# Optimization experiments

Hardware: AMD Instinct MI355X
Metric: run time of the kernel (lower is better)

The kernel has to match this reference:

```python
import jax, jax.numpy as jnp
from jax import lax
import numpy as np

VOCAB = 50000
EMBED = 300
UNITS = 512          # num_nodes[0]
D1 = 1024            # num_nodes[1]
D2 = 1024            # num_nodes[2]
NUM_CLASSES = 20
B, T = 64, 512


def setup_inputs() -> dict:
    key = jax.random.key(0)
    ks = jax.random.split(key, 12)
    s = 0.02
    return {
        "tokens": jax.random.randint(ks[0], (B, T), 0, VOCAB),
        "emb": jax.random.normal(ks[1], (VOCAB, EMBED), jnp.float32) * s,
        "Wx": jax.random.normal(ks[2], (EMBED, 4 * UNITS), jnp.float32) * s,
        "Wh": jax.random.normal(ks[3], (UNITS, 4 * UNITS), jnp.float32) * s,
        "b": jnp.zeros((4 * UNITS,), jnp.float32),
        "W1": jax.random.normal(ks[4], (UNITS, D1), jnp.float32) * s,
        "b1": jnp.zeros((D1,), jnp.float32),
        "W2": jax.random.normal(ks[5], (D1, D2), jnp.float32) * s,
        "b2": jnp.zeros((D2,), jnp.float32),
        "Wo": jax.random.normal(ks[6], (D2, NUM_CLASSES), jnp.float32) * s,
        "bo": jnp.zeros((NUM_CLASSES,), jnp.float32),
    }


def reference(tokens, emb, Wx, Wh, b, W1, b1, W2, b2, Wo, bo):
    # Embedding with mask_zero=True: token 0 timesteps are masked -> LSTM skips
    # the state update (Keras semantics).
    mask = (tokens != 0)                               # [B, T]
    x = emb[tokens]                                    # [B, T, E]
    units = Wh.shape[0]
    # Precompute input contribution to the gates (parallel over time).
    xg = jnp.einsum('bte,eg->btg', x, Wx) + b          # [B, T, 4U]

    def step(carry, inp):
        h, c = carry
        g_x, m = inp                                   # [B,4U], [B]
        g = g_x + h @ Wh                               # [B, 4U]
        i, f, cc, o = jnp.split(g, 4, axis=-1)         # Keras gate order i,f,c,o
        i = jax.nn.sigmoid(i)
        f = jax.nn.sigmoid(f)
        o = jax.nn.sigmoid(o)
        # activation='relu' replaces tanh in candidate and output transform.
        c_new = f * c + i * jax.nn.relu(cc)
        h_new = o * jax.nn.relu(c_new)
        m = m[:, None]
        h = jnp.where(m, h_new, h)
        c = jnp.where(m, c_new, c)
        return (h, c), None

    h0 = jnp.zeros((tokens.shape[0], units), x.dtype)
    (h, _), _ = lax.scan(step, (h0, h0),
                         (jnp.swapaxes(xg, 0, 1), mask.T))  # scan over T

    h = jax.nn.relu(h @ W1 + b1)
    h = jax.nn.relu(h @ W2 + b2)
    return jax.nn.softmax(h @ Wo + bo)
```

## Files before the change

### kernel.cpp

```cpp
#include <hip/hip_runtime.h>
#include <hip/hip_bf16.h>

#define B_   64
#define T_   512
#define E_   300
#define U_   512
#define G4_  2048
#define D1_  1024
#define D2_  1024
#define NC_  20
#define KP_  320

#define NBG_ 16
#define NUS_ 16
#define WH_OFF   0
#define WH_BYTES (128 * 520 * 2)
#define HS_OFF   (WH_OFF + WH_BYTES)
#define HS_BYTES (4 * 520 * 2)
#define GB_OFF   (HS_OFF + HS_BYTES)
#define GB_BYTES (4 * 128 * 4)
#define MK_OFF   (GB_OFF + GB_BYTES)
#define MK_BYTES (4 * 16 * 4)
#define SMEM_TOTAL (MK_OFF + MK_BYTES)

typedef __bf16 bf16x8 __attribute__((ext_vector_type(8)));
typedef float  f32x4  __attribute__((ext_vector_type(4)));

__device__ __forceinline__ float sigmoidf_(float x) { return 1.0f / (1.0f + __expf(-x)); }

__device__ __forceinline__ void gl_lds16(const void* g, void* l) {
    __builtin_amdgcn_global_load_lds(
        (const __attribute__((address_space(1))) unsigned int*)g,
        (__attribute__((address_space(3))) unsigned int*)l, 16, 0, 0);
}

__global__ void init_kernel(uint4* __restrict__ hch) {
    int idx = blockIdx.x * 256 + threadIdx.x;
    int bg = idx >> 9, c = idx & 511;
    hch[((size_t)bg * 2) * 512 + c] = (uint4){0u, 0u, 0u, 0u};
}

__global__ __launch_bounds__(256) void prep_wxT(const float* __restrict__ Wx,
                                                __hip_bfloat16* __restrict__ wxT) {
    __shared__ __hip_bfloat16 t[64][65];
    const int n0 = blockIdx.x * 64;
    const int k0 = blockIdx.y * 64;
    const int tid = threadIdx.x;
    for (int i = tid; i < 4096; i += 256) {
        int r = i >> 6, c = i & 63;
        int k = k0 + r;
        float v = (k < E_) ? Wx[(size_t)k * G4_ + n0 + c] : 0.f;
        t[r][c] = __float2bfloat16(v);
    }
    __syncthreads();
    for (int i = tid; i < 4096; i += 256) {
        int r = i >> 6, c = i & 63;
        wxT[(size_t)(n0 + r) * KP_ + k0 + c] = t[c][r];
    }
}

__global__ __launch_bounds__(256) void prep_xb(const int* __restrict__ tokens,
                                               const float* __restrict__ emb,
                                               __hip_bfloat16* __restrict__ xb) {
    const int row = blockIdx.x * 4 + (threadIdx.x >> 6);
    const int ln  = threadIdx.x & 63;
    const int tok = tokens[row];
    const float* src = emb + (size_t)tok * E_;
    __hip_bfloat16* dst = xb + (size_t)row * KP_;
    for (int k = ln; k < KP_; k += 64)
        dst[k] = (k < E_) ? __float2bfloat16(src[k]) : __float2bfloat16(0.f);
}

__global__ __launch_bounds__(256) void xg_gemm(const __hip_bfloat16* __restrict__ xb,
                                               const __hip_bfloat16* __restrict__ wxT,
                                               const float* __restrict__ bias,
                                               __hip_bfloat16* __restrict__ xg) {
    const int n0g = blockIdx.x * 128;
    const int bt0 = blockIdx.y * 128;
    const int tid = threadIdx.x;
    const int w   = tid >> 6;
    const int ln  = tid & 63;
    const int fn  = ln & 15;
    const int quad = ln >> 4;
    const int m0  = (w >> 1) * 64;
    const int n0w = (w & 1) * 64;

    __shared__ __align__(16) __hip_bfloat16 As[128 * 32];
    __shared__ __align__(16) __hip_bfloat16 Bs[128 * 32];

    f32x4 acc[4][4];
    #pragma unroll
    for (int im = 0; im < 4; ++im)
        #pragma unroll
        for (int in = 0; in < 4; ++in)
            acc[im][in] = (f32x4){0.f, 0.f, 0.f, 0.f};

    const __hip_bfloat16* ga = xb  + (size_t)(bt0 + w * 32 + (ln >> 2)) * KP_ + (ln & 3) * 8;
    const __hip_bfloat16* gb = wxT + (size_t)(n0g + w * 32 + (ln >> 2)) * KP_ + (ln & 3) * 8;

    for (int kt = 0; kt < KP_ / 32; ++kt) {
        gl_lds16(ga,             &As[(w * 32) * 32]);
        gl_lds16(ga + 16 * KP_,  &As[(w * 32 + 16) * 32]);
        gl_lds16(gb,             &Bs[(w * 32) * 32]);
        gl_lds16(gb + 16 * KP_,  &Bs[(w * 32 + 16) * 32]);
        ga += 32; gb += 32;
        __syncthreads();

        bf16x8 af[4], bfr[4];
        #pragma unroll
        for (int im = 0; im < 4; ++im)
            af[im] = *(const bf16x8*)&As[(m0 + im * 16 + fn) * 32 + quad * 8];
        #pragma unroll
        for (int in = 0; in < 4; ++in)
            bfr[in] = *(const bf16x8*)&Bs[(n0w + in * 16 + fn) * 32 + quad * 8];
        #pragma unroll
        for (int im = 0; im < 4; ++im)
            #pragma unroll
            for (int in = 0; in < 4; ++in)
                acc[im][in] = __builtin_amdgcn_mfma_f32_16x16x32_bf16(
                    af[im], bfr[in], acc[im][in], 0, 0, 0);
        __syncthreads();
    }

    #pragma unroll
    for (int in = 0; in < 4; ++in) {
        const int n = n0g + n0w + in * 16 + fn;
        const float bv = bias[n];
        #pragma unroll
        for (int im = 0; im < 4; ++im) {
            #pragma unroll
            for (int r = 0; r < 4; ++r) {
                int m = bt0 + m0 + im * 16 + quad * 4 + r;
                int bb = m >> 9, tt = m & 511;
                xg[(size_t)(tt * B_ + bb) * G4_ + n] =
                    __float2bfloat16(acc[im][in][r] + bv);
            }
        }
    }
}

__global__ __launch_bounds__(256, 1) void lstm_kernel(const __hip_bfloat16* __restrict__ xg,
                                                      const int* __restrict__ tokens,
                                                      const float* __restrict__ Wh,
                                                      uint4* __restrict__ hch,
                                                      __hip_bfloat16* __restrict__ hfin) {
    extern __shared__ char smem[];
    __hip_bfloat16 (*whsT)[520] = (__hip_bfloat16(*)[520])(smem + WH_OFF);
    __hip_bfloat16 (*hs)[520]   = (__hip_bfloat16(*)[520])(smem + HS_OFF);
    float (*gbuf)[128]          = (float(*)[128])(smem + GB_OFF);
    unsigned (*masks)[16]       = (unsigned(*)[16])(smem + MK_OFF);

    const int tid  = threadIdx.x;
    const int w    = tid >> 6;
    const int lane = tid & 63;
    const int fn   = lane & 15;
    const int quad = lane >> 4;
    const int us   = blockIdx.x & 15;
    const int bg   = blockIdx.x >> 4;

    for (int idx = tid; idx < 128 * 512; idx += 256) {
        int lc = idx & 127, k = idx >> 7;
        int gcol = ((lc >> 5) << 9) + us * 32 + (lc & 31);
        whsT[lc][k] = __float2bfloat16(Wh[(size_t)k * G4_ + gcol]);
    }
    if (tid < 64) {
        int b = tid >> 4, wi = tid & 15;
        const int4* tp = (const int4*)(tokens + (size_t)(bg * 4 + b) * T_ + wi * 32);
        unsigned bits = 0;
        #pragma unroll
        for (int q = 0; q < 8; ++q) {
            int4 v = tp[q];
            bits |= (v.x != 0 ? 1u : 0u) << (q * 4 + 0);
            bits |= (v.y != 0 ? 1u : 0u) << (q * 4 + 1);
            bits |= (v.z != 0 ? 1u : 0u) << (q * 4 + 2);
            bits |= (v.w != 0 ? 1u : 0u) << (q * 4 + 3);
        }
        masks[b][wi] = bits;
    }
    __syncthreads();

    const int lc0 = w * 32 + fn;
    bf16x8 wfr0[16], wfr1[16];
    #pragma unroll
    for (int kk = 0; kk < 16; ++kk) {
        wfr0[kk] = *(const bf16x8*)&whsT[lc0][kk * 32 + quad * 8];
        wfr1[kk] = *(const bf16x8*)&whsT[lc0 + 16][kk * 32 + quad * 8];
    }

    float cst[4] = {0.f, 0.f, 0.f, 0.f};
    float hst[4] = {0.f, 0.f, 0.f, 0.f};
    const int ub = tid >> 3;
    const int uj = tid & 7;

    for (int s = 0; s < T_; ++s) {
        f32x4 acc0 = (f32x4){0.f, 0.f, 0.f, 0.f};
        f32x4 acc1 = (f32x4){0.f, 0.f, 0.f, 0.f};
        if (quad == 0) {
            const __hip_bfloat16* xp =
                xg + (size_t)(s * B_ + bg * 4) * G4_ + w * 512 + us * 32 + fn;
            #pragma unroll
            for (int r = 0; r < 4; ++r) {
                acc0[r] = __bfloat162float(xp[(size_t)r * G4_]);
                acc1[r] = __bfloat162float(xp[(size_t)r * G4_ + 16]);
            }
        }

        {
            const uint4* cp = hch + ((size_t)bg * 2 + (s & 1)) * 512;
            const uint4* a0 = cp + tid;
            const uint4* a1 = cp + tid + 256;
            uint4 v0, v1;
            asm volatile(
                "global_load_dwordx4 %0, %2, off sc0 sc1\n\t"
                "global_load_dwordx4 %1, %3, off sc0 sc1\n\t"
                "s_waitcnt vmcnt(0)"
                : "=&v"(v0), "=&v"(v1) : "v"(a0), "v"(a1) : "memory");
            const unsigned exp = (unsigned)s;
            while (!((v0.y == exp) & (v0.w == exp))) {
                __builtin_amdgcn_s_sleep(1);
                asm volatile(
                    "global_load_dwordx4 %0, %1, off sc0 sc1\n\t"
                    "s_waitcnt vmcnt(0)"
                    : "=&v"(v0) : "v"(a0) : "memory");
            }
            while (!((v1.y == exp) & (v1.w == exp))) {
                __builtin_amdgcn_s_sleep(1);
                asm volatile(
                    "global_load_dwordx4 %0, %1, off sc0 sc1\n\t"
                    "s_waitcnt vmcnt(0)"
                    : "=&v"(v1) : "v"(a1) : "memory");
            }
            int c0 = tid, c1 = tid + 256;
            *(uint2*)&hs[c0 >> 7][(c0 & 127) * 4] = (uint2){v0.x, v0.z};
            *(uint2*)&hs[c1 >> 7][(c1 & 127) * 4] = (uint2){v1.x, v1.z};
        }
        __syncthreads();

        #pragma unroll
        for (int kk = 0; kk < 16; ++kk) {
            bf16x8 afr = *(const bf16x8*)&hs[fn & 3][kk * 32 + quad * 8];
            acc0 = __builtin_amdgcn_mfma_f32_16x16x32_bf16(afr, wfr0[kk], acc0, 0, 0, 0);
            acc1 = __builtin_amdgcn_mfma_f32_16x16x32_bf16(afr, wfr1[kk], acc1, 0, 0, 0);
        }
        if (quad == 0) {
            #pragma unroll
            for (int r = 0; r < 4; ++r) {
                gbuf[r][lc0]      = acc0[r];
                gbuf[r][lc0 + 16] = acc1[r];
            }
        }
        __syncthreads();

        if (tid < 32) {
            const unsigned mk = masks[ub][s >> 5] >> (s & 31) & 1u;
            #pragma unroll
            for (int q = 0; q < 4; ++q) {
                int u = uj * 4 + q;
                float gi = sigmoidf_(gbuf[ub][u]);
                float gf = sigmoidf_(gbuf[ub][32 + u]);
                float gc = gbuf[ub][64 + u];
                float go = sigmoidf_(gbuf[ub][96 + u]);
                float cn = gf * cst[q] + gi * fmaxf(gc, 0.f);
                float hn = go * fmaxf(cn, 0.f);
                if (mk) { cst[q] = cn; hst[q] = hn; }
            }
            __hip_bfloat162 p0, p1;
            p0.x = __float2bfloat16(hst[0]); p0.y = __float2bfloat16(hst[1]);
            p1.x = __float2bfloat16(hst[2]); p1.y = __float2bfloat16(hst[3]);
            unsigned d0, d1;
            __builtin_memcpy(&d0, &p0, 4);
            __builtin_memcpy(&d1, &p1, 4);
            const unsigned long long tagw = (unsigned long long)(unsigned)(s + 1) << 32;
            unsigned long long* dst = (unsigned long long*)
                (hch + ((size_t)bg * 2 + ((s + 1) & 1)) * 512 + ub * 128 + us * 8 + uj);
            __hip_atomic_store(dst,     tagw | d0, __ATOMIC_RELAXED, __HIP_MEMORY_SCOPE_AGENT);
            __hip_atomic_store(dst + 1, tagw | d1, __ATOMIC_RELAXED, __HIP_MEMORY_SCOPE_AGENT);
            if (s == T_ - 1)
                *(uint2*)&hfin[(size_t)(bg * 4 + ub) * U_ + us * 32 + uj * 4] =
                    (uint2){d0, d1};
        }
    }
}

__global__ __launch_bounds__(256) void fc1_kernel(const __hip_bfloat16* __restrict__ h,
                                                  const float* __restrict__ W,
                                                  const float* __restrict__ bias,
                                                  float* __restrict__ y) {
    int b = blockIdx.x >> 2, ch = blockIdx.x & 3;
    __shared__ float xrow[U_];
    for (int i = threadIdx.x; i < U_; i += 256)
        xrow[i] = __bfloat162float(h[b * U_ + i]);
    __syncthreads();
    int n = ch * 256 + threadIdx.x;
    float acc = 0.f;
    #pragma unroll 4
    for (int k = 0; k < U_; ++k) acc = fmaf(xrow[k], W[(size_t)k * D1_ + n], acc);
    y[b * D1_ + n] = fmaxf(acc + bias[n], 0.f);
}

__global__ __launch_bounds__(256) void fc2_kernel(const float* __restrict__ x,
                                                  const float* __restrict__ W,
                                                  const float* __restrict__ bias,
                                                  float* __restrict__ y) {
    int b = blockIdx.x >> 2, ch = blockIdx.x & 3;
    __shared__ float xrow[D1_];
    for (int i = threadIdx.x; i < D1_; i += 256) xrow[i] = x[b * D1_ + i];
    __syncthreads();
    int n = ch * 256 + threadIdx.x;
    float acc = 0.f;
    #pragma unroll 4
    for (int k = 0; k < D1_; ++k) acc = fmaf(xrow[k], W[(size_t)k * D2_ + n], acc);
    y[b * D2_ + n] = fmaxf(acc + bias[n], 0.f);
}

__global__ __launch_bounds__(64) void out_kernel(const float* __restrict__ h2,
                                                 const float* __restrict__ Wo,
                                                 const float* __restrict__ bo,
                                                 float* __restrict__ out) {
    int b = blockIdx.x;
    __shared__ float xrow[D2_];
    __shared__ float lg[NC_];
    __shared__ float red[2];
    for (int i = threadIdx.x; i < D2_; i += 64) xrow[i] = h2[b * D2_ + i];
    __syncthreads();
    if (threadIdx.x < NC_) {
        float a = bo[threadIdx.x];
        for (int k = 0; k < D2_; ++k) a = fmaf(xrow[k], Wo[k * NC_ + threadIdx.x], a);
        lg[threadIdx.x] = a;
    }
    __syncthreads();
    if (threadIdx.x == 0) {
        float mx = lg[0];
        for (int c = 1; c < NC_; ++c) mx = fmaxf(mx, lg[c]);
        float sm = 0.f;
        for (int c = 0; c < NC_; ++c) sm += expf(lg[c] - mx);
        red[0] = mx; red[1] = 1.0f / sm;
    }
    __syncthreads();
    if (threadIdx.x < NC_)
        out[b * NC_ + threadIdx.x] = expf(lg[threadIdx.x] - red[0]) * red[1];
}

extern "C" void kernel_launch(void* const* d_in, const int* in_sizes, int n_in,
                              void* d_out, int out_size, void* d_ws, size_t ws_size,
                              hipStream_t stream) {
    const int*   tokens = (const int*)d_in[0];
    const float* emb    = (const float*)d_in[1];
    const float* Wx     = (const float*)d_in[2];
    const float* Wh     = (const float*)d_in[3];
    const float* b      = (const float*)d_in[4];
    const float* W1     = (const float*)d_in[5];
    const float* b1     = (const float*)d_in[6];
    const float* W2     = (const float*)d_in[7];
    const float* b2     = (const float*)d_in[8];
    const float* Wo     = (const float*)d_in[9];
    const float* bo     = (const float*)d_in[10];
    float* out = (float*)d_out;

    char* ws = (char*)d_ws;
    const size_t XG_BYTES  = (size_t)T_ * B_ * G4_ * 2;
    const size_t CH_BYTES  = (size_t)NBG_ * 2 * 512 * 16;
    const size_t HF_BYTES  = (size_t)B_ * U_ * 2;
    __hip_bfloat16* xg   = (__hip_bfloat16*)ws;
    uint4* hch           = (uint4*)(ws + XG_BYTES);
    __hip_bfloat16* hfin = (__hip_bfloat16*)(ws + XG_BYTES + CH_BYTES);
    char* p = ws + XG_BYTES + CH_BYTES + HF_BYTES;
    float* h1            = (float*)p;                 p += (size_t)B_ * D1_ * 4;
    float* h2            = (float*)p;                 p += (size_t)B_ * D2_ * 4;
    __hip_bfloat16* xb   = (__hip_bfloat16*)p;        p += (size_t)B_ * T_ * KP_ * 2;
    __hip_bfloat16* wxT  = (__hip_bfloat16*)p;

    hipFuncSetAttribute((const void*)lstm_kernel,
                        hipFuncAttributeMaxDynamicSharedMemorySize, SMEM_TOTAL);

    init_kernel<<<32, 256, 0, stream>>>(hch);
    prep_wxT<<<dim3(32, 5), 256, 0, stream>>>(Wx, wxT);
    prep_xb<<<(B_ * T_) / 4, 256, 0, stream>>>(tokens, emb, xb);
    xg_gemm<<<dim3(16, 256), 256, 0, stream>>>(xb, wxT, b, xg);
    lstm_kernel<<<256, 256, SMEM_TOTAL, stream>>>(xg, tokens, Wh, hch, hfin);
    fc1_kernel<<<256, 256, 0, stream>>>(hfin, W1, b1, h1);
    fc2_kernel<<<256, 256, 0, stream>>>(h1, W2, b2, h2);
    out_kernel<<<64, 64, 0, stream>>>(h2, Wo, bo, out);
}
```

Measured before the change: 1.664 ms.

## Pack step tags into bf16 sign bits and replace block barriers with LDS counters

The recurrent h exchange now packs four bf16 h values per 8-byte word and stores a 4-bit step tag in their sign bits. This works because h is non-negative after relu times sigmoid, and it halves the global polling traffic. The two per-step __syncthreads are replaced by per-k-slice LDS arrival counters, so the MFMA k-loop can start on slices that have already arrived. Wh columns are permuted so each wave computes its own gate nonlinearities through lane shuffles, which removes the gbuf round trip, and the init kernel is dropped. The risks are the short 4-bit tag aliasing with stale or uninitialized workspace contents, and more spin-waiting on LDS atomics.

```diff
diff --git a/kernel.cpp b/kernel.cpp
--- a/kernel.cpp
+++ b/kernel.cpp
@@ -12,16 +12,15 @@
 #define KP_  320
 
 #define NBG_ 16
-#define NUS_ 16
 #define WH_OFF   0
 #define WH_BYTES (128 * 520 * 2)
 #define HS_OFF   (WH_OFF + WH_BYTES)
-#define HS_BYTES (4 * 520 * 2)
-#define GB_OFF   (HS_OFF + HS_BYTES)
-#define GB_BYTES (4 * 128 * 4)
-#define MK_OFF   (GB_OFF + GB_BYTES)
+#define HS_BYTES (2 * 4 * 520 * 2)
+#define MK_OFF   (HS_OFF + HS_BYTES)
 #define MK_BYTES (4 * 16 * 4)
-#define SMEM_TOTAL (MK_OFF + MK_BYTES)
+#define DN_OFF   (MK_OFF + MK_BYTES)
+#define DN_BYTES (16 * 4)
+#define SMEM_TOTAL (DN_OFF + DN_BYTES)
 
 typedef __bf16 bf16x8 __attribute__((ext_vector_type(8)));
 typedef float  f32x4  __attribute__((ext_vector_type(4)));
@@ -34,10 +33,19 @@
         (__attribute__((address_space(3))) unsigned int*)l, 16, 0, 0);
 }
 
-__global__ void init_kernel(uint4* __restrict__ hch) {
-    int idx = blockIdx.x * 256 + threadIdx.x;
-    int bg = idx >> 9, c = idx & 511;
-    hch[((size_t)bg * 2) * 512 + c] = (uint4){0u, 0u, 0u, 0u};
+__device__ __forceinline__ unsigned long long coh_load8(const unsigned long long* p) {
+    uint2 v;
+    asm volatile("global_load_dwordx2 %0, %1, off sc0 sc1\n\t"
+                 "s_waitcnt vmcnt(0)"
+                 : "=&v"(v) : "v"(p) : "memory");
+    unsigned long long r;
+    __builtin_memcpy(&r, &v, 8);
+    return r;
+}
+
+__device__ __forceinline__ unsigned tag4_(unsigned long long v) {
+    return (unsigned)(((v >> 15) & 1ull) | ((v >> 30) & 2ull) |
+                      ((v >> 45) & 4ull) | ((v >> 60) & 8ull));
 }
 
 __global__ __launch_bounds__(256) void prep_wxT(const float* __restrict__ Wx,
@@ -142,13 +150,13 @@
 __global__ __launch_bounds__(256, 1) void lstm_kernel(const __hip_bfloat16* __restrict__ xg,
                                                       const int* __restrict__ tokens,
                                                       const float* __restrict__ Wh,
-                                                      uint4* __restrict__ hch,
+                                                      unsigned long long* __restrict__ hch,
                                                       __hip_bfloat16* __restrict__ hfin) {
     extern __shared__ char smem[];
     __hip_bfloat16 (*whsT)[520] = (__hip_bfloat16(*)[520])(smem + WH_OFF);
-    __hip_bfloat16 (*hs)[520]   = (__hip_bfloat16(*)[520])(smem + HS_OFF);
-    float (*gbuf)[128]          = (float(*)[128])(smem + GB_OFF);
+    unsigned short* hsb         = (unsigned short*)(smem + HS_OFF);
     unsigned (*masks)[16]       = (unsigned(*)[16])(smem + MK_OFF);
+    int* done                   = (int*)(smem + DN_OFF);
 
     const int tid  = threadIdx.x;
     const int w    = tid >> 6;
@@ -160,7 +168,11 @@
 
     for (int idx = tid; idx < 128 * 512; idx += 256) {
         int lc = idx & 127, k = idx >> 7;
-        int gcol = ((lc >> 5) << 9) + us * 32 + (lc & 31);
+        int ww = lc >> 5, r = lc & 31;
+        int half = r >> 4, f = r & 15;
+        int g = half * 2 + (f >> 3);
+        int u = ww * 8 + (f & 7);
+        int gcol = g * 512 + us * 32 + u;
         whsT[lc][k] = __float2bfloat16(Wh[(size_t)k * G4_ + gcol]);
     }
     if (tid < 64) {
@@ -177,6 +189,8 @@
         }
         masks[b][wi] = bits;
     }
+    for (int i = tid; i < 2 * 4 * 520; i += 256) hsb[i] = 0;
+    if (tid < 16) done[tid] = 32;
     __syncthreads();
 
     const int lc0 = w * 32 + fn;
@@ -189,95 +203,124 @@
 
     float cst[4] = {0.f, 0.f, 0.f, 0.f};
     float hst[4] = {0.f, 0.f, 0.f, 0.f};
-    const int ub = tid >> 3;
-    const int uj = tid & 7;
+
+    const int sl0 = tid >> 5;
+    const int sl1 = 8 + (tid >> 5);
+    unsigned long long* chbase = hch + (size_t)bg * 2 * 512;
+    const unsigned long long* cp0 = chbase + tid;
+    const unsigned long long* cp1 = chbase + tid + 256;
+
+    const int xc0 = (fn >> 3) * 512 + us * 32 + w * 8 + (fn & 7);
+    const int xc1 = xc0 + 1024;
 
     for (int s = 0; s < T_; ++s) {
+        const int p = s & 1;
+        unsigned short* hsu = hsb + p * (4 * 520);
+
+        float xv0[4], xv1[4];
+        if (quad == 0) {
+            const __hip_bfloat16* xp = xg + (size_t)(s * B_ + bg * 4) * G4_;
+            #pragma unroll
+            for (int r = 0; r < 4; ++r) {
+                xv0[r] = __bfloat162float(xp[(size_t)r * G4_ + xc0]);
+                xv1[r] = __bfloat162float(xp[(size_t)r * G4_ + xc1]);
+            }
+        }
+
+        if (s > 0) {
+            const unsigned exp4 = (unsigned)s & 0xFu;
+            const unsigned long long* a0 = cp0 + p * 512;
+            const unsigned long long* a1 = cp1 + p * 512;
+            unsigned long long v0, v1;
+            {
+                uint2 t0, t1;
+                asm volatile(
+                    "global_load_dwordx2 %0, %2, off sc0 sc1\n\t"
+                    "global_load_dwordx2 %1, %3, off sc0 sc1\n\t"
+                    "s_waitcnt vmcnt(0)"
+                    : "=&v"(t0), "=&v"(t1) : "v"(a0), "v"(a1) : "memory");
+                __builtin_memcpy(&v0, &t0, 8);
+                __builtin_memcpy(&v1, &t1, 8);
+            }
+            while (tag4_(v0) != exp4) {
+                __builtin_amdgcn_s_sleep(1);
+                v0 = coh_load8(a0);
+            }
+            {
+                unsigned long long pl = v0 & 0x7FFF7FFF7FFF7FFFull;
+                hsu[0 * 520 + tid] = (unsigned short)(pl);
+                hsu[1 * 520 + tid] = (unsigned short)(pl >> 16);
+                hsu[2 * 520 + tid] = (unsigned short)(pl >> 32);
+                hsu[3 * 520 + tid] = (unsigned short)(pl >> 48);
+            }
+            __hip_atomic_fetch_add(&done[sl0], 1, __ATOMIC_RELEASE,
+                                   __HIP_MEMORY_SCOPE_WORKGROUP);
+            while (tag4_(v1) != exp4) {
+                __builtin_amdgcn_s_sleep(1);
+                v1 = coh_load8(a1);
+            }
+            {
+                unsigned long long pl = v1 & 0x7FFF7FFF7FFF7FFFull;
+                hsu[0 * 520 + tid + 256] = (unsigned short)(pl);
+                hsu[1 * 520 + tid + 256] = (unsigned short)(pl >> 16);
+                hsu[2 * 520 + tid + 256] = (unsigned short)(pl >> 32);
+                hsu[3 * 520 + tid + 256] = (unsigned short)(pl >> 48);
+            }
+            __hip_atomic_fetch_add(&done[sl1], 1, __ATOMIC_RELEASE,
+                                   __HIP_MEMORY_SCOPE_WORKGROUP);
+        }
+
         f32x4 acc0 = (f32x4){0.f, 0.f, 0.f, 0.f};
         f32x4 acc1 = (f32x4){0.f, 0.f, 0.f, 0.f};
         if (quad == 0) {
-            const __hip_bfloat16* xp =
-                xg + (size_t)(s * B_ + bg * 4) * G4_ + w * 512 + us * 32 + fn;
+            #pragma unroll
+            for (int r = 0; r < 4; ++r) { acc0[r] = xv0[r]; acc1[r] = xv1[r]; }
+        }
+        const int thr = 32 * (s + 1);
+        #pragma unroll
+        for (int ks = 0; ks < 16; ++ks) {
+            while (__hip_atomic_load(&done[ks], __ATOMIC_ACQUIRE,
+                                     __HIP_MEMORY_SCOPE_WORKGROUP) < thr)
+                __builtin_amdgcn_s_sleep(1);
+            bf16x8 afr = *(const bf16x8*)&hsu[(fn & 3) * 520 + ks * 32 + quad * 8];
+            acc0 = __builtin_amdgcn_mfma_f32_16x16x32_bf16(afr, wfr0[ks], acc0, 0, 0, 0);
+            acc1 = __builtin_amdgcn_mfma_f32_16x16x32_bf16(afr, wfr1[ks], acc1, 0, 0, 0);
+        }
+
+        const int j = lane & 7;
+        const unsigned tag = (unsigned)(s + 1) & 0xFu;
+        #pragma unroll
+        for (int r = 0; r < 4; ++r) {
+            float gi = __shfl(acc0[r], j, 64);
+            float gf = __shfl(acc0[r], j + 8, 64);
+            float gc = __shfl(acc1[r], j, 64);
+            float go = __shfl(acc1[r], j + 8, 64);
+            if (lane < 8) {
+                float cn = sigmoidf_(gf) * cst[r] + sigmoidf_(gi) * fmaxf(gc, 0.f);
+                float hn = sigmoidf_(go) * fmaxf(cn, 0.f);
+                unsigned mk = (masks[r][s >> 5] >> (s & 31)) & 1u;
+                if (mk) { cst[r] = cn; hst[r] = hn; }
+            }
+        }
+        if (lane < 8) {
+            unsigned long long outv = 0;
             #pragma unroll
             for (int r = 0; r < 4; ++r) {
-                acc0[r] = __bfloat162float(xp[(size_t)r * G4_]);
-                acc1[r] = __bfloat162float(xp[(size_t)r * G4_ + 16]);
-            }
-        }
-
-        {
-            const uint4* cp = hch + ((size_t)bg * 2 + (s & 1)) * 512;
-            const uint4* a0 = cp + tid;
-            const uint4* a1 = cp + tid + 256;
-            uint4 v0, v1;
-            asm volatile(
-                "global_load_dwordx4 %0, %2, off sc0 sc1\n\t"
-                "global_load_dwordx4 %1, %3, off sc0 sc1\n\t"
-                "s_waitcnt vmcnt(0)"
-                : "=&v"(v0), "=&v"(v1) : "v"(a0), "v"(a1) : "memory");
-            const unsigned exp = (unsigned)s;
-            while (!((v0.y == exp) & (v0.w == exp))) {
-                __builtin_amdgcn_s_sleep(1);
-                asm volatile(
-                    "global_load_dwordx4 %0, %1, off sc0 sc1\n\t"
-                    "s_waitcnt vmcnt(0)"
-                    : "=&v"(v0) : "v"(a0) : "memory");
-            }
-            while (!((v1.y == exp) & (v1.w == exp))) {
-                __builtin_amdgcn_s_sleep(1);
-                asm volatile(
-                    "global_load_dwordx4 %0, %1, off sc0 sc1\n\t"
-                    "s_waitcnt vmcnt(0)"
-                    : "=&v"(v1) : "v"(a1) : "memory");
-            }
-            int c0 = tid, c1 = tid + 256;
-            *(uint2*)&hs[c0 >> 7][(c0 & 127) * 4] = (uint2){v0.x, v0.z};
-            *(uint2*)&hs[c1 >> 7][(c1 & 127) * 4] = (uint2){v1.x, v1.z};
-        }
-        __syncthreads();
-
-        #pragma unroll
-        for (int kk = 0; kk < 16; ++kk) {
-            bf16x8 afr = *(const bf16x8*)&hs[fn & 3][kk * 32 + quad * 8];
-            acc0 = __builtin_amdgcn_mfma_f32_16x16x32_bf16(afr, wfr0[kk], acc0, 0, 0, 0);
-            acc1 = __builtin_amdgcn_mfma_f32_16x16x32_bf16(afr, wfr1[kk], acc1, 0, 0, 0);
-        }
-        if (quad == 0) {
-            #pragma unroll
-            for (int r = 0; r < 4; ++r) {
-                gbuf[r][lc0]      = acc0[r];
-                gbuf[r][lc0 + 16] = acc1[r];
-            }
-        }
-        __syncthreads();
-
-        if (tid < 32) {
-            const unsigned mk = masks[ub][s >> 5] >> (s & 31) & 1u;
-            #pragma unroll
-            for (int q = 0; q < 4; ++q) {
-                int u = uj * 4 + q;
-                float gi = sigmoidf_(gbuf[ub][u]);
-                float gf = sigmoidf_(gbuf[ub][32 + u]);
-                float gc = gbuf[ub][64 + u];
-                float go = sigmoidf_(gbuf[ub][96 + u]);
-                float cn = gf * cst[q] + gi * fmaxf(gc, 0.f);
-                float hn = go * fmaxf(cn, 0.f);
-                if (mk) { cst[q] = cn; hst[q] = hn; }
-            }
-            __hip_bfloat162 p0, p1;
-            p0.x = __float2bfloat16(hst[0]); p0.y = __float2bfloat16(hst[1]);
-            p1.x = __float2bfloat16(hst[2]); p1.y = __float2bfloat16(hst[3]);
-            unsigned d0, d1;
-            __builtin_memcpy(&d0, &p0, 4);
-            __builtin_memcpy(&d1, &p1, 4);
-            const unsigned long long tagw = (unsigned long long)(unsigned)(s + 1) << 32;
-            unsigned long long* dst = (unsigned long long*)
-                (hch + ((size_t)bg * 2 + ((s + 1) & 1)) * 512 + ub * 128 + us * 8 + uj);
-            __hip_atomic_store(dst,     tagw | d0, __ATOMIC_RELAXED, __HIP_MEMORY_SCOPE_AGENT);
-            __hip_atomic_store(dst + 1, tagw | d1, __ATOMIC_RELAXED, __HIP_MEMORY_SCOPE_AGENT);
-            if (s == T_ - 1)
-                *(uint2*)&hfin[(size_t)(bg * 4 + ub) * U_ + us * 32 + uj * 4] =
-                    (uint2){d0, d1};
+                __hip_bfloat16 hb = __float2bfloat16(hst[r]);
+                unsigned short bits;
+                __builtin_memcpy(&bits, &hb, 2);
+                bits |= (unsigned short)(((tag >> r) & 1u) << 15);
+                outv |= (unsigned long long)bits << (16 * r);
+            }
+            unsigned long long* dst =
+                chbase + ((s + 1) & 1) * 512 + us * 32 + w * 8 + lane;
+            __hip_atomic_store(dst, outv, __ATOMIC_RELAXED, __HIP_MEMORY_SCOPE_AGENT);
+            if (s == T_ - 1) {
+                #pragma unroll
+                for (int r = 0; r < 4; ++r)
+                    hfin[(size_t)(bg * 4 + r) * U_ + us * 32 + w * 8 + lane] =
+                        __float2bfloat16(hst[r]);
+            }
         }
     }
 }
@@ -359,21 +402,21 @@
 
     char* ws = (char*)d_ws;
     const size_t XG_BYTES  = (size_t)T_ * B_ * G4_ * 2;
-    const size_t CH_BYTES  = (size_t)NBG_ * 2 * 512 * 16;
+    const size_t CH_BYTES  = (size_t)NBG_ * 2 * 512 * 8;
     const size_t HF_BYTES  = (size_t)B_ * U_ * 2;
-    __hip_bfloat16* xg   = (__hip_bfloat16*)ws;
-    uint4* hch           = (uint4*)(ws + XG_BYTES);
-    __hip_bfloat16* hfin = (__hip_bfloat16*)(ws + XG_BYTES + CH_BYTES);
+    __hip_bfloat16* xg       = (__hip_bfloat16*)ws;
+    unsigned long long* hch  = (unsigned long long*)(ws + XG_BYTES);
+    __hip_bfloat16* hfin     = (__hip_bfloat16*)(ws + XG_BYTES + CH_BYTES);
     char* p = ws + XG_BYTES + CH_BYTES + HF_BYTES;
     float* h1            = (float*)p;                 p += (size_t)B_ * D1_ * 4;
     float* h2            = (float*)p;                 p += (size_t)B_ * D2_ * 4;
     __hip_bfloat16* xb   = (__hip_bfloat16*)p;        p += (size_t)B_ * T_ * KP_ * 2;
     __hip_bfloat16* wxT  = (__hip_bfloat16*)p;
 
+
     hipFuncSetAttribute((const void*)lstm_kernel,
                         hipFuncAttributeMaxDynamicSharedMemorySize, SMEM_TOTAL);
 
-    init_kernel<<<32, 256, 0, stream>>>(hch);
     prep_wxT<<<dim3(32, 5), 256, 0, stream>>>(Wx, wxT);
     prep_xb<<<(B_ * T_) / 4, 256, 0, stream>>>(tokens, emb, xb);
     xg_gemm<<<dim3(16, 256), 256, 0, stream>>>(xb, wxT, b, xg);
```

New measurement: 2.049 ms. +23.2%, slower.
